# Kernel optimization log

Measured on AMD Instinct MI355X. Metric: run time of the kernel, lower is better.

## Reference

```python
import jax, jax.numpy as jnp
import numpy as np

N_R, N_U, N_P = 40000, 30000, 30000
N = N_R + N_U + N_P
E = 1600000
NFEAT, NHID, NCLASS = 128, 128, 40


def setup_inputs() -> dict:
    key = jax.random.key(0)
    ks = jax.random.split(key, 12)
    s = 0.05
    return {
        "inputx_r": jax.random.normal(ks[0], (N_R, 5), jnp.float32),
        "inputx_u": jax.random.normal(ks[1], (N_U, 7), jnp.float32),
        "inputx_p": jax.random.normal(ks[2], (N_P, 6), jnp.float32),
        "edge_index": jax.random.randint(ks[3], (2, E), 0, N, jnp.int64)
            if jax.config.jax_enable_x64 else jax.random.randint(ks[3], (2, E), 0, N, jnp.int32),
        "W_r": jax.random.normal(ks[4], (5, NFEAT), jnp.float32) * s,
        "b_r": jax.random.normal(ks[5], (NFEAT,), jnp.float32) * s,
        "W_u": jax.random.normal(ks[6], (7, NFEAT), jnp.float32) * s,
        "b_u": jax.random.normal(ks[7], (NFEAT,), jnp.float32) * s,
        "W_p": jax.random.normal(ks[8], (6, NFEAT), jnp.float32) * s,
        "b_p": jax.random.normal(ks[9], (NFEAT,), jnp.float32) * s,
        "W1": jax.random.normal(ks[10], (NFEAT, NHID), jnp.float32) * s,
        "W2": jax.random.normal(ks[11], (NHID, NCLASS), jnp.float32) * s,
    }


def _gcn_conv(x, W, src, dst, num_nodes):
    # GCNConv(add_self_loops=False, normalize=False, bias=False):
    # out = A @ (x @ W), unit edge weights, aggregation at dst of source messages.
    h = x @ W                                      # [N, d_out]
    return jax.ops.segment_sum(h[src], dst, num_segments=num_nodes)


def reference(inputx_r, inputx_u, inputx_p, edge_index,
              W_r, b_r, W_u, b_u, W_p, b_p, W1, W2):
    # Segment-wise input projections (nums = [[N_R, N_R+N_U], [.,.], [.,.]]
    # with empty 2nd/3rd blocks; tail is the p-segment), then two GCN layers.
    x = jnp.concatenate([
        inputx_r @ W_r + b_r,   # nodes [0 : N_R]
        inputx_u @ W_u + b_u,   # nodes [N_R : N_R+N_U]
        inputx_p @ W_p + b_p,   # nodes [N_R+N_U : N]
    ], axis=0)                  # [N, NFEAT]
    src, dst = edge_index[0], edge_index[1]
    h = jax.nn.relu(_gcn_conv(x, W1, src, dst, N))   # gc1 + relu
    # dropout: inference (training=False) -> identity
    out = _gcn_conv(h, W2, src, dst, N)              # gc2
    return out
```

## Files before the change

kernel.cpp:

```cpp
#include <hip/hip_runtime.h>

constexpr int kNR = 40000;
constexpr int kNU = 30000;
constexpr int kNP = 30000;
constexpr int kN  = 100000;
constexpr int kE  = 1600000;
constexpr int kF  = 128;
constexpr int kC  = 40;
constexpr int kBN = 64;
constexpr int kNB = (kN + kBN - 1) / kBN;
constexpr int kNBp = 1600;
constexpr int kSlot = 2048;
constexpr int kPackB = 98;
constexpr int kFuseB = kPackB;
constexpr int kW2B   = kPackB + 1;
constexpr int kScat0 = kPackB + 2;
constexpr int kScatB = 256;
constexpr int kCE    = kE / kScatB;
constexpr int kEPT   = (kCE + 1023) / 1024;
constexpr int kPrepB = kScat0 + kScatB;

typedef __attribute__((ext_vector_type(8))) short bf16x8;
typedef __attribute__((ext_vector_type(4))) float f32x4;

__device__ __forceinline__ float bf_to_f(unsigned short h) {
    union { unsigned int i; float f; } u; u.i = ((unsigned int)h) << 16; return u.f;
}
__device__ __forceinline__ unsigned short f_to_bf(float f) {
    union { unsigned int i; float f; } u; u.f = f;
    unsigned int r = u.i + 0x7FFFu + ((u.i >> 16) & 1u);
    return (unsigned short)(r >> 16);
}
__device__ __forceinline__ float2 bf2_to_f2(unsigned int p) {
    union { unsigned int i; float f; } lo, hi;
    lo.i = (p & 0xFFFFu) << 16;
    hi.i = p & 0xFFFF0000u;
    return make_float2(lo.f, hi.f);
}
__device__ __forceinline__ unsigned int pack_bf2(float a, float b) {
    return (unsigned int)f_to_bf(a) | ((unsigned int)f_to_bf(b) << 16);
}
__device__ __forceinline__ float ldf(const void* p, int i, int isbf) {
    return isbf ? bf_to_f(((const unsigned short*)p)[i]) : ((const float*)p)[i];
}
__device__ __forceinline__ int lde(const int* p, int i, int is64) {
    return is64 ? p[2 * i] : p[i];
}

__device__ __forceinline__ int sniff_isbf(const void* W1, int t, int* sh) {
    if (t < 64) {
        unsigned int wv = ((const unsigned int*)W1)[t];
        unsigned int ax = wv & 0x7FFFu;
        int pl = (ax == 0u) || (ax > 0x2000u && ax < 0x4000u);
        unsigned long long mk = __ballot(pl);
        if (t == 0) *sh = (__popcll(mk) >= 48) ? 1 : 0;
    }
    __syncthreads();
    return *sh;
}

__global__ void __launch_bounds__(1024) gcn_prep(
        const void* __restrict__ xr, const void* __restrict__ xu, const void* __restrict__ xp,
        const void* __restrict__ Wr, const void* __restrict__ br,
        const void* __restrict__ Wu, const void* __restrict__ bu,
        const void* __restrict__ Wp, const void* __restrict__ bp,
        const void* __restrict__ W1, const void* __restrict__ W2,
        const int* __restrict__ ei,
        unsigned short* __restrict__ fwfrag, unsigned short* __restrict__ w2frag,
        uint4* __restrict__ xpack, int* __restrict__ gcnt,
        unsigned int* __restrict__ slots) {
    __shared__ __align__(16) char smem[29696];
    __shared__ int sflag;
    int t = threadIdx.x;
    int bx = blockIdx.x;
    if (bx < kPackB) {
        int isbf = sniff_isbf(W1, t, &sflag);
        int n = bx * 1024 + t;
        if (n >= kN) return;
        const void* base; int roff, d;
        if (n < kNR)            { base = xr; roff = n * 5;               d = 5; }
        else if (n < kNR + kNU) { base = xu; roff = (n - kNR) * 7;       d = 7; }
        else                    { base = xp; roff = (n - kNR - kNU) * 6; d = 6; }
        float f[8];
        #pragma unroll
        for (int i = 0; i < 8; i++) f[i] = (i < d) ? ldf(base, roff + i, isbf) : 0.f;
        uint4 u;
        u.x = pack_bf2(f[0], f[1]);  u.y = pack_bf2(f[2], f[3]);
        u.z = pack_bf2(f[4], f[5]);  u.w = pack_bf2(f[6], f[7]);
        xpack[n] = u;
    } else if (bx == kFuseB) {
        int isbf = sniff_isbf(W1, t, &sflag);
        float* sw   = (float*)smem;
        float* pacc = (float*)(smem + 10752);
        unsigned short* flds = (unsigned short*)(smem + 21504);
        for (int i = t; i < 21 * kF; i += 1024) {
            int r = i >> 7, c = i & 127;
            float v;
            if (r < 5)        v = ldf(Wr, r * kF + c, isbf);
            else if (r < 12)  v = ldf(Wu, (r - 5) * kF + c, isbf);
            else if (r < 18)  v = ldf(Wp, (r - 12) * kF + c, isbf);
            else if (r == 18) v = ldf(br, c, isbf);
            else if (r == 19) v = ldf(bu, c, isbf);
            else              v = ldf(bp, c, isbf);
            sw[i] = v;
        }
        __syncthreads();
        {
            bool active = (t < 256);
            int j = t & 127, half = (t >> 7) & 1;
            float acc[21];
            #pragma unroll
            for (int r = 0; r < 21; r++) acc[r] = 0.f;
            if (active) {
                int k0 = half * 64, k1 = k0 + 64;
                for (int k = k0; k < k1; k++) {
                    float w1 = ldf(W1, k * kF + j, isbf);
                    #pragma unroll
                    for (int r = 0; r < 21; r++) acc[r] += sw[r * kF + k] * w1;
                }
            }
            if (active && half == 1) {
                #pragma unroll
                for (int r = 0; r < 21; r++) pacc[r * kF + j] = acc[r];
            }
            __syncthreads();
            if (active && half == 0) {
                #pragma unroll
                for (int r = 0; r < 21; r++) acc[r] += pacc[r * kF + j];
                unsigned short row[32];
                #pragma unroll
                for (int s = 0; s < 32; s++) row[s] = 0;
                #pragma unroll
                for (int i = 0; i < 5; i++) row[0  + i] = f_to_bf(acc[i]);
                #pragma unroll
                for (int i = 0; i < 7; i++) row[8  + i] = f_to_bf(acc[5 + i]);
                #pragma unroll
                for (int i = 0; i < 6; i++) row[16 + i] = f_to_bf(acc[12 + i]);
                row[24] = f_to_bf(acc[18]);  row[25] = f_to_bf(acc[19]);  row[26] = f_to_bf(acc[20]);
                #pragma unroll
                for (int s = 0; s < 32; s++) flds[j * 32 + s] = row[s];
            }
        }
        __syncthreads();
        for (int idx = t; idx < 8 * 64; idx += 1024) {
            int t8 = idx >> 6, lane = idx & 63;
            int mm = lane & 15, q = lane >> 4;
            #pragma unroll
            for (int j = 0; j < 8; j++)
                fwfrag[idx * 8 + j] = flds[(16 * t8 + mm) * 32 + q * 8 + j];
        }
    } else if (bx == kW2B) {
        int isbf = sniff_isbf(W1, t, &sflag);
        for (int idx = t; idx < 12 * 64; idx += 1024) {
            int st = idx >> 6, lane = idx & 63;
            int s = st / 3, tt = st % 3;
            int mm = lane & 15, q = lane >> 4;
            int cls = 16 * tt + mm;
            #pragma unroll
            for (int j = 0; j < 8; j++) {
                int k = s * 32 + q * 8 + j;
                w2frag[idx * 8 + j] = (cls < kC) ? f_to_bf(ldf(W2, k * kC + cls, isbf))
                                                 : (unsigned short)0;
            }
        }
    } else {
        int* hist = (int*)smem;
        int* cur  = (int*)(smem + 6400);
        if (t < 64) {
            int v = ((const int*)ei)[2 * t + 1];
            unsigned long long mk = __ballot(v != 0);
            if (t == 0) sflag = (mk == 0ull) ? 1 : 0;
        }
        for (int i = t; i < kNBp; i += 1024) hist[i] = 0;
        __syncthreads();
        int is64 = sflag;
        int blk = bx - kScat0;
        int e0 = blk * kCE, e1 = e0 + kCE;
        unsigned int dv[kEPT], sv[kEPT];
        #pragma unroll
        for (int it = 0; it < kEPT; it++) {
            int e = e0 + t + it * 1024;
            bool ok = (e < e1);
            dv[it] = ok ? (unsigned int)lde(ei, kE + e, is64) : 0xFFFFFFFFu;
            sv[it] = ok ? (unsigned int)lde(ei, e, is64) : 0u;
        }
        #pragma unroll
        for (int it = 0; it < kEPT; it++)
            if (dv[it] < (unsigned int)kN) atomicAdd(&hist[dv[it] >> 6], 1);
        __syncthreads();
        int off = (blk * 401) % kNBp;
        for (int j = t; j < kNBp; j += 1024) {
            int i = j + off;
            if (i >= kNBp) i -= kNBp;
            int h = hist[i];
            cur[i] = (h > 0) ? atomicAdd(&gcnt[i], h) : 0;
        }
        __syncthreads();
        #pragma unroll
        for (int it = 0; it < kEPT; it++) {
            if (dv[it] < (unsigned int)kN) {
                unsigned int sval = (sv[it] < (unsigned int)kN) ? sv[it] : 0u;
                int b = (int)(dv[it] >> 6);
                int pos = atomicAdd(&cur[b], 1);
                if (pos < kSlot) slots[(size_t)b * kSlot + pos] = (sval << 6) | (dv[it] & 63u);
            }
        }
    }
}

__global__ void __launch_bounds__(256) GCN_2190433321521_kernel(
        const unsigned int* __restrict__ slots,
        const int* __restrict__ gcnt,
        const uint4* __restrict__ xpack,
        const unsigned short* __restrict__ fwfrag,
        const unsigned short* __restrict__ w2frag,
        int* __restrict__ rpb,
        int* __restrict__ rpe,
        int* __restrict__ col,
        unsigned short* __restrict__ hw) {
    __shared__ __align__(16) char smem[25600];
    float*          agg_l  = (float*)smem;
    int*            cnt_l  = (int*)(smem + 7424);
    int*            strt_l = (int*)(smem + 7680);
    int*            cntv_l = (int*)(smem + 7936);
    unsigned int*   wst    = (unsigned int*)(smem + 8192);
    int*            col_l  = (int*)(smem + 16384);
    unsigned short* hbuf   = (unsigned short*)(smem + 8192);
    unsigned short* cst    = (unsigned short*)smem;

    int b = blockIdx.x;
    int base = b * kBN;
    int nn = min(kBN, kN - base);
    int tid = threadIdx.x;

    if (tid < kBN) cnt_l[tid] = 0;
    __syncthreads();
    int p0 = b * kSlot;
    int m = min(gcnt[b], kSlot);
    int p1 = p0 + m;

    for (int ib = p0 + tid; ib < p1; ib += 1024) {
        unsigned int w[4]; int ok[4];
        #pragma unroll
        for (int j = 0; j < 4; j++) {
            int i = ib + j * 256;
            ok[j] = (i < p1);
            w[j] = ok[j] ? slots[i] : 0u;
        }
        #pragma unroll
        for (int j = 0; j < 4; j++) {
            int i = ib + j * 256;
            if (ok[j]) {
                wst[i - p0] = w[j];
                atomicAdd(&cnt_l[w[j] & 63u], 1);
            }
        }
    }
    __syncthreads();
    if (tid < 64) {
        int v = cnt_l[tid];
        int incl = v;
        #pragma unroll
        for (int o = 1; o < 64; o <<= 1) {
            int y = __shfl_up(incl, o, 64);
            if (tid >= o) incl += y;
        }
        int cursor = p0 + incl - v;
        cnt_l[tid]  = cursor;
        strt_l[tid] = cursor;
        cntv_l[tid] = v;
        if (tid < nn) { rpb[base + tid] = cursor; rpe[base + tid] = cursor + v; }
    }
    __syncthreads();

    for (int i = p0 + tid; i < p1; i += 256) {
        unsigned int w = wst[i - p0];
        unsigned int s = w >> 6;
        int dloc = (int)(w & 63u);
        int pos = atomicAdd(&cnt_l[dloc], 1);
        col_l[pos - p0] = (int)s;
    }
    __syncthreads();
    for (int i = tid; i < m; i += 256) col[p0 + i] = col_l[i];

    {
        int node = tid >> 2, j = tid & 3;
        float aR[8], aU[8], aP[8];
        #pragma unroll
        for (int i = 0; i < 8; i++) { aR[i] = 0.f; aU[i] = 0.f; aP[i] = 0.f; }
        float cR = 0.f, cU = 0.f, cP = 0.f;
        int start = strt_l[node] - p0;
        int iend = start + cntv_l[node];
        int i = start + j;
        int sN = (i < iend) ? col_l[i] : -1;
        uint4 uN = make_uint4(0u, 0u, 0u, 0u);
        if (sN >= 0) uN = xpack[sN];
        while (sN >= 0) {
            int s = sN; uint4 u = uN;
            i += 4;
            sN = (i < iend) ? col_l[i] : -1;
            if (sN >= 0) uN = xpack[sN];
            float2 q0 = bf2_to_f2(u.x), q1 = bf2_to_f2(u.y);
            float2 q2 = bf2_to_f2(u.z), q3 = bf2_to_f2(u.w);
            if (s < kNR) {
                aR[0]+=q0.x; aR[1]+=q0.y; aR[2]+=q1.x; aR[3]+=q1.y;
                aR[4]+=q2.x; aR[5]+=q2.y; aR[6]+=q3.x; aR[7]+=q3.y; cR += 1.f;
            } else if (s < kNR + kNU) {
                aU[0]+=q0.x; aU[1]+=q0.y; aU[2]+=q1.x; aU[3]+=q1.y;
                aU[4]+=q2.x; aU[5]+=q2.y; aU[6]+=q3.x; aU[7]+=q3.y; cU += 1.f;
            } else {
                aP[0]+=q0.x; aP[1]+=q0.y; aP[2]+=q1.x; aP[3]+=q1.y;
                aP[4]+=q2.x; aP[5]+=q2.y; aP[6]+=q3.x; aP[7]+=q3.y; cP += 1.f;
            }
        }
        #pragma unroll
        for (int i2 = 0; i2 < 8; i2++) {
            float v = aR[i2];
            v += __shfl_xor(v, 1, 64);  v += __shfl_xor(v, 2, 64);
            if (j == 0) agg_l[node * 29 + i2] = v;
        }
        #pragma unroll
        for (int i2 = 0; i2 < 8; i2++) {
            float v = aU[i2];
            v += __shfl_xor(v, 1, 64);  v += __shfl_xor(v, 2, 64);
            if (j == 0) agg_l[node * 29 + 8 + i2] = v;
        }
        #pragma unroll
        for (int i2 = 0; i2 < 8; i2++) {
            float v = aP[i2];
            v += __shfl_xor(v, 1, 64);  v += __shfl_xor(v, 2, 64);
            if (j == 0) agg_l[node * 29 + 16 + i2] = v;
        }
        float v = cR;
        v += __shfl_xor(v, 1, 64);  v += __shfl_xor(v, 2, 64);
        if (j == 0) agg_l[node * 29 + 24] = v;
        v = cU;
        v += __shfl_xor(v, 1, 64);  v += __shfl_xor(v, 2, 64);
        if (j == 0) agg_l[node * 29 + 25] = v;
        v = cP;
        v += __shfl_xor(v, 1, 64);  v += __shfl_xor(v, 2, 64);
        if (j == 0) agg_l[node * 29 + 26] = v;
    }
    __syncthreads();

    int wid = tid >> 6, lane = tid & 63;
    int mm = lane & 15, q = lane >> 4;
    int node = wid * 16 + mm;
    bf16x8 a1;
    #pragma unroll
    for (int j = 0; j < 8; j++) {
        int sl = q * 8 + j;
        a1[j] = (sl < 27) ? (short)f_to_bf(agg_l[node * 29 + sl]) : (short)0;
    }
    __syncthreads();
    const bf16x8* fwf = (const bf16x8*)fwfrag;
    f32x4 c1[8];
    #pragma unroll
    for (int t = 0; t < 8; t++) {
        f32x4 z = {0.f, 0.f, 0.f, 0.f};
        c1[t] = __builtin_amdgcn_mfma_f32_16x16x32_bf16(a1, fwf[t * 64 + lane], z, 0, 0, 0);
    }
    unsigned short* hb = hbuf + wid * 16 * 136;
    #pragma unroll
    for (int t = 0; t < 8; t++) {
        #pragma unroll
        for (int r = 0; r < 4; r++)
            hb[(q * 4 + r) * 136 + 16 * t + mm] = f_to_bf(fmaxf(c1[t][r], 0.f));
    }
    const bf16x8* w2f = (const bf16x8*)w2frag;
    f32x4 c2[3];
    #pragma unroll
    for (int t = 0; t < 3; t++) { c2[t].x = 0.f; c2[t].y = 0.f; c2[t].z = 0.f; c2[t].w = 0.f; }
    #pragma unroll
    for (int s = 0; s < 4; s++) {
        bf16x8 a2 = *(const bf16x8*)&hb[mm * 136 + s * 32 + q * 8];
        #pragma unroll
        for (int t = 0; t < 3; t++)
            c2[t] = __builtin_amdgcn_mfma_f32_16x16x32_bf16(a2, w2f[(s * 3 + t) * 64 + lane],
                                                            c2[t], 0, 0, 0);
    }
    #pragma unroll
    for (int t = 0; t < 3; t++) {
        int cls = 16 * t + mm;
        if (cls < kC) {
            #pragma unroll
            for (int r = 0; r < 4; r++)
                cst[(wid * 16 + q * 4 + r) * kC + cls] = f_to_bf(c2[t][r]);
        }
    }
    __syncthreads();
    {
        int tot = nn * (kC / 2);
        const unsigned int* cs32 = (const unsigned int*)cst;
        unsigned int* ho = (unsigned int*)(hw + (size_t)base * kC);
        for (int i = tid; i < tot; i += 256) ho[i] = cs32[i];
    }
}

__global__ void __launch_bounds__(256) gcn_gather2(const unsigned int* __restrict__ hw32,
                                                   const int* __restrict__ rpb,
                                                   const int* __restrict__ rpe,
                                                   const int* __restrict__ col,
                                                   unsigned int* __restrict__ out,
                                                   const void* __restrict__ W1) {
    __shared__ int sisbf;
    int t = threadIdx.x;
    int isbf = sniff_isbf(W1, t, &sisbf);
    int w = (blockIdx.x * 256 + t) >> 6;
    if (w >= kN) return;
    int lane = t & 63;
    int grp = lane / 5;
    int cp  = lane % 5;
    int beg = rpb[w], end = rpe[w];
    float f0 = 0.f, f1 = 0.f, f2 = 0.f, f3 = 0.f, f4 = 0.f, f5 = 0.f, f6 = 0.f, f7 = 0.f;
    if (grp < 12) {
        const uint4* hp = (const uint4*)hw32;
        auto acc = [&](uint4 u) {
            float2 a0 = bf2_to_f2(u.x), a1 = bf2_to_f2(u.y);
            float2 a2 = bf2_to_f2(u.z), a3 = bf2_to_f2(u.w);
            f0 += a0.x; f1 += a0.y; f2 += a1.x; f3 += a1.y;
            f4 += a2.x; f5 += a2.y; f6 += a3.x; f7 += a3.y;
        };
        int e = beg + grp;
        int c0 = (e      < end) ? col[e]      : -1;
        int c1 = (e + 12 < end) ? col[e + 12] : -1;
        if (c0 >= 0) acc(hp[(size_t)c0 * 5 + cp]);
        if (c1 >= 0) acc(hp[(size_t)c1 * 5 + cp]);
        for (e += 24; e < end; e += 12) acc(hp[(size_t)col[e] * 5 + cp]);
    }
    f0 += __shfl(f0, lane + 30, 64);  f1 += __shfl(f1, lane + 30, 64);
    f2 += __shfl(f2, lane + 30, 64);  f3 += __shfl(f3, lane + 30, 64);
    f4 += __shfl(f4, lane + 30, 64);  f5 += __shfl(f5, lane + 30, 64);
    f6 += __shfl(f6, lane + 30, 64);  f7 += __shfl(f7, lane + 30, 64);
    f0 += __shfl(f0, lane + 15, 64);  f1 += __shfl(f1, lane + 15, 64);
    f2 += __shfl(f2, lane + 15, 64);  f3 += __shfl(f3, lane + 15, 64);
    f4 += __shfl(f4, lane + 15, 64);  f5 += __shfl(f5, lane + 15, 64);
    f6 += __shfl(f6, lane + 15, 64);  f7 += __shfl(f7, lane + 15, 64);
    f0 += __shfl(f0, lane + 5, 64) + __shfl(f0, lane + 10, 64);
    f1 += __shfl(f1, lane + 5, 64) + __shfl(f1, lane + 10, 64);
    f2 += __shfl(f2, lane + 5, 64) + __shfl(f2, lane + 10, 64);
    f3 += __shfl(f3, lane + 5, 64) + __shfl(f3, lane + 10, 64);
    f4 += __shfl(f4, lane + 5, 64) + __shfl(f4, lane + 10, 64);
    f5 += __shfl(f5, lane + 5, 64) + __shfl(f5, lane + 10, 64);
    f6 += __shfl(f6, lane + 5, 64) + __shfl(f6, lane + 10, 64);
    f7 += __shfl(f7, lane + 5, 64) + __shfl(f7, lane + 10, 64);
    if (lane < 5) {
        if (isbf) {
            uint4 o;
            o.x = pack_bf2(f0, f1);  o.y = pack_bf2(f2, f3);
            o.z = pack_bf2(f4, f5);  o.w = pack_bf2(f6, f7);
            ((uint4*)out)[(size_t)w * 5 + lane] = o;
        } else {
            float4* of = (float4*)out;
            of[(size_t)w * 10 + 2 * lane]     = make_float4(f0, f1, f2, f3);
            of[(size_t)w * 10 + 2 * lane + 1] = make_float4(f4, f5, f6, f7);
        }
    }
}

extern "C" void kernel_launch(void* const* d_in, const int* in_sizes, int n_in,
                              void* d_out, int out_size, void* d_ws, size_t ws_size,
                              hipStream_t stream) {
    const void* xr = d_in[0];
    const void* xu = d_in[1];
    const void* xp = d_in[2];
    const int*  ei = (const int*)d_in[3];
    const void* Wr = d_in[4];
    const void* br = d_in[5];
    const void* Wu = d_in[6];
    const void* bu = d_in[7];
    const void* Wp = d_in[8];
    const void* bp = d_in[9];
    const void* W1 = d_in[10];
    const void* W2 = d_in[11];
    (void)in_sizes; (void)n_in; (void)out_size; (void)ws_size;

    char* ws = (char*)d_ws;
    size_t off = 0;
    auto alloc = [&](size_t bytes) -> void* {
        void* p = (void*)(ws + off);
        off = (off + bytes + 255) & ~(size_t)255;
        return p;
    };
    int*            gcnt   = (int*)           alloc((size_t)kNBp * 4);
    unsigned short* fwfrag = (unsigned short*)alloc(8 * 64 * 8 * 2);
    unsigned short* w2frag = (unsigned short*)alloc(12 * 64 * 8 * 2);
    uint4*          xpack  = (uint4*)         alloc((size_t)kN * 16);
    unsigned int*   slots  = (unsigned int*)  alloc((size_t)kNB * kSlot * 4);
    int*            col    = (int*)           alloc((size_t)kNB * kSlot * 4);
    int*            rpb    = (int*)           alloc((size_t)kN * 4);
    int*            rpe    = (int*)           alloc((size_t)kN * 4);
    unsigned short* hwb    = (unsigned short*)alloc((size_t)kN * kC * 2);

    hipMemsetAsync(gcnt, 0, (size_t)kNBp * 4, stream);
    gcn_prep<<<kPrepB, 1024, 0, stream>>>(xr, xu, xp, Wr, br, Wu, bu, Wp, bp, W1, W2,
                                          ei, fwfrag, w2frag, xpack, gcnt, slots);
    GCN_2190433321521_kernel<<<kNB, 256, 0, stream>>>(slots, gcnt, xpack, fwfrag, w2frag,
                                                      rpb, rpe, col, hwb);
    gcn_gather2<<<(kN * 64 + 255) / 256, 256, 0, stream>>>((const unsigned int*)hwb, rpb, rpe,
                                                           col, (unsigned int*)d_out, W1);
}
```

Before: 188.1 us.

## Split layer-2 features into 8 column planes for cache-local gather

Result: slower. 214.4 us (+14.0%).

```diff
diff --git a/kernel.cpp b/kernel.cpp
--- a/kernel.cpp
+++ b/kernel.cpp
@@ -19,6 +19,11 @@
 constexpr int kCE    = kE / kScatB;
 constexpr int kEPT   = (kCE + 1023) / 1024;
 constexpr int kPrepB = kScat0 + kScatB;
+constexpr int kPl  = 8;
+constexpr int kPC  = 5;
+constexpr int kNPB = 256;
+constexpr int kGBn = (kN + kNPB - 1) / kNPB;
+constexpr int kGB  = kPl * kGBn;
 
 typedef __attribute__((ext_vector_type(8))) short bf16x8;
 typedef __attribute__((ext_vector_type(4))) float f32x4;
@@ -217,7 +222,7 @@
         int* __restrict__ rpb,
         int* __restrict__ rpe,
         int* __restrict__ col,
-        unsigned short* __restrict__ hw) {
+        uint4* __restrict__ hpl) {
     __shared__ __align__(16) char smem[25600];
     float*          agg_l  = (float*)smem;
     int*            cnt_l  = (int*)(smem + 7424);
@@ -290,16 +295,10 @@
         for (int i = 0; i < 8; i++) { aR[i] = 0.f; aU[i] = 0.f; aP[i] = 0.f; }
         float cR = 0.f, cU = 0.f, cP = 0.f;
         int start = strt_l[node] - p0;
-        int iend = start + cntv_l[node];
-        int i = start + j;
-        int sN = (i < iend) ? col_l[i] : -1;
-        uint4 uN = make_uint4(0u, 0u, 0u, 0u);
-        if (sN >= 0) uN = xpack[sN];
-        while (sN >= 0) {
-            int s = sN; uint4 u = uN;
-            i += 4;
-            sN = (i < iend) ? col_l[i] : -1;
-            if (sN >= 0) uN = xpack[sN];
+        int c = cntv_l[node];
+        for (int i = start + j; i < start + c; i += 4) {
+            int s = col_l[i];
+            uint4 u = xpack[s];
             float2 q0 = bf2_to_f2(u.x), q1 = bf2_to_f2(u.y);
             float2 q2 = bf2_to_f2(u.z), q3 = bf2_to_f2(u.w);
             if (s < kNR) {
@@ -389,71 +388,61 @@
         }
     }
     __syncthreads();
-    {
-        int tot = nn * (kC / 2);
-        const unsigned int* cs32 = (const unsigned int*)cst;
-        unsigned int* ho = (unsigned int*)(hw + (size_t)base * kC);
-        for (int i = tid; i < tot; i += 256) ho[i] = cs32[i];
-    }
-}
-
-__global__ void __launch_bounds__(256) gcn_gather2(const unsigned int* __restrict__ hw32,
+    for (int idx = tid; idx < kPl * kBN; idx += 256) {
+        int p = idx >> 6, i = idx & 63;
+        if (i < nn) {
+            const unsigned short* cr = &cst[i * kC + p * kPC];
+            uint4 v;
+            v.x = (unsigned)cr[0] | ((unsigned)cr[1] << 16);
+            v.y = (unsigned)cr[2] | ((unsigned)cr[3] << 16);
+            v.z = (unsigned)cr[4];
+            v.w = 0u;
+            hpl[(size_t)p * kN + base + i] = v;
+        }
+    }
+}
+
+__global__ void __launch_bounds__(256) gcn_gather2(const uint4* __restrict__ hpl,
                                                    const int* __restrict__ rpb,
                                                    const int* __restrict__ rpe,
                                                    const int* __restrict__ col,
-                                                   unsigned int* __restrict__ out,
+                                                   void* __restrict__ out,
                                                    const void* __restrict__ W1) {
     __shared__ int sisbf;
     int t = threadIdx.x;
     int isbf = sniff_isbf(W1, t, &sisbf);
-    int w = (blockIdx.x * 256 + t) >> 6;
-    if (w >= kN) return;
-    int lane = t & 63;
-    int grp = lane / 5;
-    int cp  = lane % 5;
-    int beg = rpb[w], end = rpe[w];
-    float f0 = 0.f, f1 = 0.f, f2 = 0.f, f3 = 0.f, f4 = 0.f, f5 = 0.f, f6 = 0.f, f7 = 0.f;
-    if (grp < 12) {
-        const uint4* hp = (const uint4*)hw32;
-        auto acc = [&](uint4 u) {
-            float2 a0 = bf2_to_f2(u.x), a1 = bf2_to_f2(u.y);
-            float2 a2 = bf2_to_f2(u.z), a3 = bf2_to_f2(u.w);
-            f0 += a0.x; f1 += a0.y; f2 += a1.x; f3 += a1.y;
-            f4 += a2.x; f5 += a2.y; f6 += a3.x; f7 += a3.y;
-        };
-        int e = beg + grp;
-        int c0 = (e      < end) ? col[e]      : -1;
-        int c1 = (e + 12 < end) ? col[e + 12] : -1;
-        if (c0 >= 0) acc(hp[(size_t)c0 * 5 + cp]);
-        if (c1 >= 0) acc(hp[(size_t)c1 * 5 + cp]);
-        for (e += 24; e < end; e += 12) acc(hp[(size_t)col[e] * 5 + cp]);
-    }
-    f0 += __shfl(f0, lane + 30, 64);  f1 += __shfl(f1, lane + 30, 64);
-    f2 += __shfl(f2, lane + 30, 64);  f3 += __shfl(f3, lane + 30, 64);
-    f4 += __shfl(f4, lane + 30, 64);  f5 += __shfl(f5, lane + 30, 64);
-    f6 += __shfl(f6, lane + 30, 64);  f7 += __shfl(f7, lane + 30, 64);
-    f0 += __shfl(f0, lane + 15, 64);  f1 += __shfl(f1, lane + 15, 64);
-    f2 += __shfl(f2, lane + 15, 64);  f3 += __shfl(f3, lane + 15, 64);
-    f4 += __shfl(f4, lane + 15, 64);  f5 += __shfl(f5, lane + 15, 64);
-    f6 += __shfl(f6, lane + 15, 64);  f7 += __shfl(f7, lane + 15, 64);
-    f0 += __shfl(f0, lane + 5, 64) + __shfl(f0, lane + 10, 64);
-    f1 += __shfl(f1, lane + 5, 64) + __shfl(f1, lane + 10, 64);
-    f2 += __shfl(f2, lane + 5, 64) + __shfl(f2, lane + 10, 64);
-    f3 += __shfl(f3, lane + 5, 64) + __shfl(f3, lane + 10, 64);
-    f4 += __shfl(f4, lane + 5, 64) + __shfl(f4, lane + 10, 64);
-    f5 += __shfl(f5, lane + 5, 64) + __shfl(f5, lane + 10, 64);
-    f6 += __shfl(f6, lane + 5, 64) + __shfl(f6, lane + 10, 64);
-    f7 += __shfl(f7, lane + 5, 64) + __shfl(f7, lane + 10, 64);
-    if (lane < 5) {
-        if (isbf) {
-            uint4 o;
-            o.x = pack_bf2(f0, f1);  o.y = pack_bf2(f2, f3);
-            o.z = pack_bf2(f4, f5);  o.w = pack_bf2(f6, f7);
-            ((uint4*)out)[(size_t)w * 5 + lane] = o;
-        } else {
-            float4* of = (float4*)out;
-            of[(size_t)w * 10 + 2 * lane]     = make_float4(f0, f1, f2, f3);
-            of[(size_t)w * 10 + 2 * lane + 1] = make_float4(f4, f5, f6, f7);
+    int plane = blockIdx.x & 7;
+    int nb0 = (blockIdx.x >> 3) * kNPB;
+    const uint4* hp = hpl + (size_t)plane * kN;
+    int j = t & 3;
+    #pragma unroll
+    for (int pass = 0; pass < kNPB / 64; pass++) {
+        int n = nb0 + pass * 64 + (t >> 2);
+        if (n < kN) {
+            int beg = rpb[n], end = rpe[n];
+            float a0 = 0.f, a1 = 0.f, a2 = 0.f, a3 = 0.f, a4 = 0.f;
+            for (int e = beg + j; e < end; e += 4) {
+                int s = col[e];
+                uint4 u = hp[s];
+                float2 q0 = bf2_to_f2(u.x), q1 = bf2_to_f2(u.y);
+                a0 += q0.x; a1 += q0.y; a2 += q1.x; a3 += q1.y;
+                a4 += bf_to_f((unsigned short)(u.z & 0xFFFFu));
+            }
+            a0 += __shfl_xor(a0, 1, 64);  a0 += __shfl_xor(a0, 2, 64);
+            a1 += __shfl_xor(a1, 1, 64);  a1 += __shfl_xor(a1, 2, 64);
+            a2 += __shfl_xor(a2, 1, 64);  a2 += __shfl_xor(a2, 2, 64);
+            a3 += __shfl_xor(a3, 1, 64);  a3 += __shfl_xor(a3, 2, 64);
+            a4 += __shfl_xor(a4, 1, 64);  a4 += __shfl_xor(a4, 2, 64);
+            if (j == 0) {
+                if (isbf) {
+                    unsigned short* ob = (unsigned short*)out + (size_t)n * kC + plane * kPC;
+                    ob[0] = f_to_bf(a0);  ob[1] = f_to_bf(a1);  ob[2] = f_to_bf(a2);
+                    ob[3] = f_to_bf(a3);  ob[4] = f_to_bf(a4);
+                } else {
+                    float* of = (float*)out + (size_t)n * kC + plane * kPC;
+                    of[0] = a0;  of[1] = a1;  of[2] = a2;  of[3] = a3;  of[4] = a4;
+                }
+            }
         }
     }
 }
@@ -490,13 +479,12 @@
     int*            col    = (int*)           alloc((size_t)kNB * kSlot * 4);
     int*            rpb    = (int*)           alloc((size_t)kN * 4);
     int*            rpe    = (int*)           alloc((size_t)kN * 4);
-    unsigned short* hwb    = (unsigned short*)alloc((size_t)kN * kC * 2);
+    uint4*          hpl    = (uint4*)         alloc((size_t)kPl * kN * 16);
 
     hipMemsetAsync(gcnt, 0, (size_t)kNBp * 4, stream);
     gcn_prep<<<kPrepB, 1024, 0, stream>>>(xr, xu, xp, Wr, br, Wu, bu, Wp, bp, W1, W2,
                                           ei, fwfrag, w2frag, xpack, gcnt, slots);
     GCN_2190433321521_kernel<<<kNB, 256, 0, stream>>>(slots, gcnt, xpack, fwfrag, w2frag,
-                                                      rpb, rpe, col, hwb);
-    gcn_gather2<<<(kN * 64 + 255) / 256, 256, 0, stream>>>((const unsigned int*)hwb, rpb, rpe,
-                                                           col, (unsigned int*)d_out, W1);
-}
+                                                      rpb, rpe, col, hpl);
+    gcn_gather2<<<kGB, 256, 0, stream>>>(hpl, rpb, rpe, col, d_out, W1);
+}
```
